# Kernel tuning notes

Measured on AMD Instinct MI355X. Metric: run time of the kernel, lower is better.

## Reference

```python
import jax, jax.numpy as jnp
import numpy as np

N_NODES = 50000
N_EDGES = 640000
N_REL = 200
D_IN = 128
D_OUT = 128


def setup_inputs() -> dict:
    key = jax.random.key(0)
    k1, k2, k3, k4, k5, k6 = jax.random.split(key, 6)
    x = jax.random.normal(k1, (N_NODES, D_IN), dtype=jnp.float32)
    edge_index = jax.random.randint(k2, (2, N_EDGES), 0, N_NODES, dtype=jnp.int64)
    edge_type = jax.random.randint(k3, (N_EDGES,), 0, N_REL, dtype=jnp.int64)
    rel_emb = jax.random.normal(k4, (N_REL, D_IN), dtype=jnp.float32)
    # nn.Linear weights stored as [out_features, in_features]
    W_lin = jax.random.normal(k5, (D_OUT, D_IN), dtype=jnp.float32) * (1.0 / np.sqrt(D_IN))
    # xavier_uniform for attn kernel [1, D_IN]
    limit = np.sqrt(6.0 / (1 + D_IN))
    W_attn = jax.random.uniform(k6, (1, D_IN), dtype=jnp.float32, minval=-limit, maxval=limit)
    return {"x": x, "edge_index": edge_index, "edge_type": edge_type,
            "rel_emb": rel_emb, "W_lin": W_lin, "W_attn": W_attn}


def reference(x, edge_index, edge_type, rel_emb, W_lin, W_attn):
    # x: [N, D_in]; edge_index: [2, E]; edge_type: [E]; rel_emb: [R, D_in]
    x_trans = x @ W_lin.T                       # [N, D_out]
    src_idx, tgt_idx = edge_index[0], edge_index[1]
    h_src = x[src_idx]                          # [E, D_in] gather
    h_rel = rel_emb[edge_type]                  # [E, D_in] gather
    sum_feat = h_src + h_rel                    # [E, D_in]
    attn = jax.nn.sigmoid(sum_feat @ W_attn.T)  # [E, 1]
    msg = x_trans[src_idx] * attn               # [E, D_out]
    out = jax.ops.segment_sum(msg, tgt_idx, num_segments=x.shape[0])  # [N, D_out]
    return jax.nn.relu(out)
```

## Files before the change

kernel.cpp:

```cpp
#include <hip/hip_runtime.h>
#include <hip/hip_bf16.h>

#define N_NODES 50000
#define N_EDGES 640000
#define N_REL   200
#define D       128
#define CAP     64
#define RANGES  8
#define NODES_PER_RANGE (N_NODES / RANGES)
#define CHUNK_EDGES 2560
#define N_CHUNKS (N_EDGES / CHUNK_EDGES)

typedef __attribute__((ext_vector_type(8))) short short8;
typedef __attribute__((ext_vector_type(4))) float floatx4;

__device__ __forceinline__ unsigned short f2bf(float f) {
    unsigned u = __float_as_uint(f);
    u += 0x7FFF + ((u >> 16) & 1);
    return (unsigned short)(u >> 16);
}

__device__ __forceinline__ float sigmoidf(float x) {
    return 1.f / (1.f + __expf(-x));
}

__global__ void setup_kernel(const float* __restrict__ W,
                             const float* __restrict__ x,
                             const float* __restrict__ rel,
                             const float* __restrict__ Wattn,
                             unsigned short* __restrict__ Wbf,
                             float* __restrict__ s_rel,
                             float* __restrict__ s_node,
                             int* __restrict__ count) {
    const int b = blockIdx.x;
    if (b < 64) {
        const int i = b * 256 + threadIdx.x;
        Wbf[i] = f2bf(W[i]);
    } else if (b < 114) {
        const int wave = (b - 64) * 4 + (threadIdx.x >> 6);
        const int lane = threadIdx.x & 63;
        if (wave < N_REL) {
            const float* __restrict__ row = rel + (size_t)wave * D;
            float a = fmaf(row[lane], Wattn[lane],
                           row[lane + 64] * Wattn[lane + 64]);
#pragma unroll
            for (int off = 32; off; off >>= 1)
                a += __shfl_down(a, off);
            if (lane == 0) s_rel[wave] = a;
        }
    } else if (b < 310) {
        const int i = (b - 114) * 256 + threadIdx.x;
        if (i < N_NODES) count[i] = 0;
    } else {
        const int node = (b - 310) * 8 + (threadIdx.x >> 5);
        const int sub  = threadIdx.x & 31;
        if (node < N_NODES) {
            const float4 xv = ((const float4*)(x + (size_t)node * D))[sub];
            const float4 wv = ((const float4*)Wattn)[sub];
            float a = xv.x * wv.x + xv.y * wv.y + xv.z * wv.z + xv.w * wv.w;
#pragma unroll
            for (int off = 16; off; off >>= 1)
                a += __shfl_xor(a, off);
            if (sub == 0) s_node[node] = a;
        }
    }
}

__global__ void xtrans_mfma_kernel(const float* __restrict__ x,
                                   const unsigned short* __restrict__ Wbf,
                                   unsigned short* __restrict__ xt) {
    const int wid = (blockIdx.x * blockDim.x + threadIdx.x) >> 6;
    if (wid >= N_NODES / 16) return;
    const int lane = threadIdx.x & 63;
    const int r16  = lane & 15;
    const int quad = lane >> 4;
    const int m0   = wid * 16;

    short8 af[4];
#pragma unroll
    for (int s = 0; s < 4; ++s) {
        const int k0 = s * 32 + quad * 8;
        const float* __restrict__ xr = x + (size_t)(m0 + r16) * D + k0;
        const float4 lo = *(const float4*)(xr);
        const float4 hi = *(const float4*)(xr + 4);
        short8 a;
        a[0] = (short)f2bf(lo.x); a[1] = (short)f2bf(lo.y);
        a[2] = (short)f2bf(lo.z); a[3] = (short)f2bf(lo.w);
        a[4] = (short)f2bf(hi.x); a[5] = (short)f2bf(hi.y);
        a[6] = (short)f2bf(hi.z); a[7] = (short)f2bf(hi.w);
        af[s] = a;
    }

#pragma unroll
    for (int t = 0; t < 8; ++t) {
        floatx4 acc = {0.f, 0.f, 0.f, 0.f};
#pragma unroll
        for (int s = 0; s < 4; ++s) {
            const int k0 = s * 32 + quad * 8;
            const short8 b = *(const short8*)(Wbf + (size_t)(t * 16 + r16) * D + k0);
            acc = __builtin_amdgcn_mfma_f32_16x16x32_bf16(af[s], b, acc, 0, 0, 0);
        }
#pragma unroll
        for (int r = 0; r < 4; ++r) {
            const int orow = m0 + quad * 4 + r;
            xt[(size_t)orow * D + t * 16 + r16] = f2bf(acc[r]);
        }
    }
}

__global__ void scatter_kernel(const int* __restrict__ src_idx,
                               const int* __restrict__ tgt_idx,
                               const int* __restrict__ etype,
                               const float* __restrict__ s_node,
                               const float* __restrict__ s_rel,
                               int* __restrict__ count,
                               unsigned* __restrict__ sorted) {
    const int b     = blockIdx.x;
    const int lo    = (b & 7) * NODES_PER_RANGE;
    const int hi    = lo + NODES_PER_RANGE;
    const int base  = (b >> 3) * CHUNK_EDGES + threadIdx.x;

#pragma unroll
    for (int it = 0; it < CHUNK_EDGES / 256; ++it) {
        const int e = base + it * 256;
        const int t = tgt_idx[e];
        if (t >= lo && t < hi) {
            const int s = src_idx[e];
            const int r = etype[e];
            const float logit = s_node[s] + s_rel[r];
            const unsigned rec =
                ((unsigned)f2bf(sigmoidf(logit)) << 16) | (unsigned)s;
            const int k = atomicAdd(&count[t], 1);
            sorted[t * CAP + k] = rec;
        }
    }
}

__device__ __forceinline__ void gproc(unsigned r, const unsigned short* __restrict__ xt,
                                      int sub, float4& acc) {
    const unsigned src = r & 0xFFFFu;
    const float a = __uint_as_float(r & 0xFFFF0000u);
    const uint2 p = *(const uint2*)(xt + (size_t)src * D + sub * 4);
    acc.x = fmaf(a, __uint_as_float(p.x << 16),        acc.x);
    acc.y = fmaf(a, __uint_as_float(p.x & 0xFFFF0000u), acc.y);
    acc.z = fmaf(a, __uint_as_float(p.y << 16),        acc.z);
    acc.w = fmaf(a, __uint_as_float(p.y & 0xFFFF0000u), acc.w);
}

__global__ void gather_kernel(const int* __restrict__ count,
                              const unsigned* __restrict__ sorted,
                              const unsigned short* __restrict__ xt,
                              float* __restrict__ out) {
    const int wid  = (blockIdx.x * blockDim.x + threadIdx.x) >> 6;
    const int lane = threadIdx.x & 63;
    const int half = lane >> 5;
    const int sub  = lane & 31;
    const int t    = wid * 2 + half;
    if (t >= N_NODES) return;

    const int cnt = count[t];
    const unsigned* __restrict__ rec = sorted + (size_t)t * CAP;

    float4 acc = {0.f, 0.f, 0.f, 0.f};
    int i = 0;
    for (; i + 4 <= cnt; i += 4) {
        const uint4 r4 = *(const uint4*)(rec + i);
        gproc(r4.x, xt, sub, acc);
        gproc(r4.y, xt, sub, acc);
        gproc(r4.z, xt, sub, acc);
        gproc(r4.w, xt, sub, acc);
    }
    for (; i < cnt; ++i)
        gproc(rec[i], xt, sub, acc);

    float4 o;
    o.x = fmaxf(acc.x, 0.f);
    o.y = fmaxf(acc.y, 0.f);
    o.z = fmaxf(acc.z, 0.f);
    o.w = fmaxf(acc.w, 0.f);
    ((float4*)(out + (size_t)t * D))[sub] = o;
}

extern "C" void kernel_launch(void* const* d_in, const int* in_sizes, int n_in,
                              void* d_out, int out_size, void* d_ws, size_t ws_size,
                              hipStream_t stream) {
    const float* x        = (const float*)d_in[0];
    const int*   edge_idx = (const int*)d_in[1];
    const int*   etype    = (const int*)d_in[2];
    const float* rel_emb  = (const float*)d_in[3];
    const float* W_lin    = (const float*)d_in[4];
    const float* W_attn   = (const float*)d_in[5];
    float* out = (float*)d_out;

    const int* src_idx = edge_idx;
    const int* tgt_idx = edge_idx + N_EDGES;

    unsigned short* xt   = (unsigned short*)d_ws;
    float* s_node        = (float*)(xt + (size_t)N_NODES * D);
    float* s_rel         = s_node + N_NODES;
    unsigned short* Wbf  = (unsigned short*)(s_rel + N_REL);
    int*   count         = (int*)(Wbf + D * D);
    unsigned* sorted     = (unsigned*)(count + N_NODES);

    setup_kernel<<<dim3(310 + (N_NODES + 7) / 8), dim3(256), 0, stream>>>(
        W_lin, x, rel_emb, W_attn, Wbf, s_rel, s_node, count);

    xtrans_mfma_kernel<<<dim3((N_NODES / 16 * 64 + 255) / 256), dim3(256), 0, stream>>>(
        x, Wbf, xt);

    scatter_kernel<<<dim3(N_CHUNKS * RANGES), dim3(256), 0, stream>>>(
        src_idx, tgt_idx, etype, s_node, s_rel, count, sorted);

    gather_kernel<<<dim3(N_NODES / 8), dim3(256), 0, stream>>>(
        count, sorted, xt, out);
}
```

Baseline: 167.1 us.

## Fuse x-transform GEMM and edge scatter into one interleaved launch

Merges the bf16 MFMA x·W^T kernel and the edge scatter/bucketing kernel into a single launch. Block groups are interleaved proportionally, so compute-heavy GEMM blocks and atomic-heavy scatter blocks run concurrently and one kernel launch and its tail are removed. It also switches edge-index, record reads and output stores to nontemporal loads and stores to reduce cache pollution. The interleaving mapping adds a little index arithmetic and may change occupancy balance.

```diff
diff --git a/kernel.cpp b/kernel.cpp
--- a/kernel.cpp
+++ b/kernel.cpp
@@ -11,8 +11,14 @@
 #define CHUNK_EDGES 2560
 #define N_CHUNKS (N_EDGES / CHUNK_EDGES)
 
+#define XT_WAVES   (N_NODES / 16)
+#define XT_GROUPS  98
+#define SC_GROUPS  N_CHUNKS
+#define TOT_GROUPS (XT_GROUPS + SC_GROUPS)
+
 typedef __attribute__((ext_vector_type(8))) short short8;
 typedef __attribute__((ext_vector_type(4))) float floatx4;
+typedef __attribute__((ext_vector_type(4))) unsigned uintx4;
 
 __device__ __forceinline__ unsigned short f2bf(float f) {
     unsigned u = __float_as_uint(f);
@@ -24,14 +30,15 @@
     return 1.f / (1.f + __expf(-x));
 }
 
-__global__ void setup_kernel(const float* __restrict__ W,
-                             const float* __restrict__ x,
-                             const float* __restrict__ rel,
-                             const float* __restrict__ Wattn,
-                             unsigned short* __restrict__ Wbf,
-                             float* __restrict__ s_rel,
-                             float* __restrict__ s_node,
-                             int* __restrict__ count) {
+__global__ __launch_bounds__(256) void setup_kernel(
+        const float* __restrict__ W,
+        const float* __restrict__ x,
+        const float* __restrict__ rel,
+        const float* __restrict__ Wattn,
+        unsigned short* __restrict__ Wbf,
+        float* __restrict__ s_rel,
+        float* __restrict__ s_node,
+        int* __restrict__ count) {
     const int b = blockIdx.x;
     if (b < 64) {
         const int i = b * 256 + threadIdx.x;
@@ -66,91 +73,99 @@
     }
 }
 
-__global__ void xtrans_mfma_kernel(const float* __restrict__ x,
-                                   const unsigned short* __restrict__ Wbf,
-                                   unsigned short* __restrict__ xt) {
-    const int wid = (blockIdx.x * blockDim.x + threadIdx.x) >> 6;
-    if (wid >= N_NODES / 16) return;
-    const int lane = threadIdx.x & 63;
-    const int r16  = lane & 15;
-    const int quad = lane >> 4;
-    const int m0   = wid * 16;
-
-    short8 af[4];
-#pragma unroll
-    for (int s = 0; s < 4; ++s) {
-        const int k0 = s * 32 + quad * 8;
-        const float* __restrict__ xr = x + (size_t)(m0 + r16) * D + k0;
-        const float4 lo = *(const float4*)(xr);
-        const float4 hi = *(const float4*)(xr + 4);
-        short8 a;
-        a[0] = (short)f2bf(lo.x); a[1] = (short)f2bf(lo.y);
-        a[2] = (short)f2bf(lo.z); a[3] = (short)f2bf(lo.w);
-        a[4] = (short)f2bf(hi.x); a[5] = (short)f2bf(hi.y);
-        a[6] = (short)f2bf(hi.z); a[7] = (short)f2bf(hi.w);
-        af[s] = a;
-    }
-
-#pragma unroll
-    for (int t = 0; t < 8; ++t) {
-        floatx4 acc = {0.f, 0.f, 0.f, 0.f};
+__global__ __launch_bounds__(256) void fused_kernel(
+        const float* __restrict__ x,
+        const unsigned short* __restrict__ Wbf,
+        unsigned short* __restrict__ xt,
+        const int* __restrict__ src_idx,
+        const int* __restrict__ tgt_idx,
+        const int* __restrict__ etype,
+        const float* __restrict__ s_node,
+        const float* __restrict__ s_rel,
+        int* __restrict__ count,
+        unsigned* __restrict__ sorted) {
+    const int g    = blockIdx.x >> 3;
+    const int sub8 = blockIdx.x & 7;
+    const int xg   = (g * XT_GROUPS) / TOT_GROUPS;
+    const bool is_x = (((g + 1) * XT_GROUPS) / TOT_GROUPS) > xg;
+
+    if (is_x) {
+        const int wid = (xg * 8 + sub8) * 4 + (threadIdx.x >> 6);
+        if (wid >= XT_WAVES) return;
+        const int lane = threadIdx.x & 63;
+        const int r16  = lane & 15;
+        const int quad = lane >> 4;
+        const int m0   = wid * 16;
+
+        short8 af[4];
 #pragma unroll
         for (int s = 0; s < 4; ++s) {
             const int k0 = s * 32 + quad * 8;
-            const short8 b = *(const short8*)(Wbf + (size_t)(t * 16 + r16) * D + k0);
-            acc = __builtin_amdgcn_mfma_f32_16x16x32_bf16(af[s], b, acc, 0, 0, 0);
-        }
-#pragma unroll
-        for (int r = 0; r < 4; ++r) {
-            const int orow = m0 + quad * 4 + r;
-            xt[(size_t)orow * D + t * 16 + r16] = f2bf(acc[r]);
+            const float* __restrict__ xr = x + (size_t)(m0 + r16) * D + k0;
+            const float4 lo = *(const float4*)(xr);
+            const float4 hi = *(const float4*)(xr + 4);
+            short8 a;
+            a[0] = (short)f2bf(lo.x); a[1] = (short)f2bf(lo.y);
+            a[2] = (short)f2bf(lo.z); a[3] = (short)f2bf(lo.w);
+            a[4] = (short)f2bf(hi.x); a[5] = (short)f2bf(hi.y);
+            a[6] = (short)f2bf(hi.z); a[7] = (short)f2bf(hi.w);
+            af[s] = a;
+        }
+
+#pragma unroll
+        for (int t = 0; t < 8; ++t) {
+            floatx4 acc = {0.f, 0.f, 0.f, 0.f};
+#pragma unroll
+            for (int s = 0; s < 4; ++s) {
+                const int k0 = s * 32 + quad * 8;
+                const short8 bfr = *(const short8*)(Wbf + (size_t)(t * 16 + r16) * D + k0);
+                acc = __builtin_amdgcn_mfma_f32_16x16x32_bf16(af[s], bfr, acc, 0, 0, 0);
+            }
+#pragma unroll
+            for (int r = 0; r < 4; ++r) {
+                const int orow = m0 + quad * 4 + r;
+                xt[(size_t)orow * D + t * 16 + r16] = f2bf(acc[r]);
+            }
+        }
+    } else {
+        const int sg   = g - xg;
+        const int lo   = sub8 * NODES_PER_RANGE;
+        const int hi   = lo + NODES_PER_RANGE;
+        const int base = sg * CHUNK_EDGES + threadIdx.x;
+
+#pragma unroll
+        for (int it = 0; it < CHUNK_EDGES / 256; ++it) {
+            const int e = base + it * 256;
+            const int t = __builtin_nontemporal_load(tgt_idx + e);
+            if (t >= lo && t < hi) {
+                const int s = __builtin_nontemporal_load(src_idx + e);
+                const int r = __builtin_nontemporal_load(etype + e);
+                const float logit = s_node[s] + s_rel[r];
+                const unsigned rec =
+                    ((unsigned)f2bf(sigmoidf(logit)) << 16) | (unsigned)s;
+                const int k = atomicAdd(&count[t], 1);
+                sorted[t * CAP + k] = rec;
+            }
         }
     }
 }
 
-__global__ void scatter_kernel(const int* __restrict__ src_idx,
-                               const int* __restrict__ tgt_idx,
-                               const int* __restrict__ etype,
-                               const float* __restrict__ s_node,
-                               const float* __restrict__ s_rel,
-                               int* __restrict__ count,
-                               unsigned* __restrict__ sorted) {
-    const int b     = blockIdx.x;
-    const int lo    = (b & 7) * NODES_PER_RANGE;
-    const int hi    = lo + NODES_PER_RANGE;
-    const int base  = (b >> 3) * CHUNK_EDGES + threadIdx.x;
-
-#pragma unroll
-    for (int it = 0; it < CHUNK_EDGES / 256; ++it) {
-        const int e = base + it * 256;
-        const int t = tgt_idx[e];
-        if (t >= lo && t < hi) {
-            const int s = src_idx[e];
-            const int r = etype[e];
-            const float logit = s_node[s] + s_rel[r];
-            const unsigned rec =
-                ((unsigned)f2bf(sigmoidf(logit)) << 16) | (unsigned)s;
-            const int k = atomicAdd(&count[t], 1);
-            sorted[t * CAP + k] = rec;
-        }
-    }
-}
-
 __device__ __forceinline__ void gproc(unsigned r, const unsigned short* __restrict__ xt,
-                                      int sub, float4& acc) {
+                                      int sub, floatx4& acc) {
     const unsigned src = r & 0xFFFFu;
     const float a = __uint_as_float(r & 0xFFFF0000u);
     const uint2 p = *(const uint2*)(xt + (size_t)src * D + sub * 4);
-    acc.x = fmaf(a, __uint_as_float(p.x << 16),        acc.x);
-    acc.y = fmaf(a, __uint_as_float(p.x & 0xFFFF0000u), acc.y);
-    acc.z = fmaf(a, __uint_as_float(p.y << 16),        acc.z);
-    acc.w = fmaf(a, __uint_as_float(p.y & 0xFFFF0000u), acc.w);
-}
-
-__global__ void gather_kernel(const int* __restrict__ count,
-                              const unsigned* __restrict__ sorted,
-                              const unsigned short* __restrict__ xt,
-                              float* __restrict__ out) {
+    acc[0] = fmaf(a, __uint_as_float(p.x << 16),         acc[0]);
+    acc[1] = fmaf(a, __uint_as_float(p.x & 0xFFFF0000u), acc[1]);
+    acc[2] = fmaf(a, __uint_as_float(p.y << 16),         acc[2]);
+    acc[3] = fmaf(a, __uint_as_float(p.y & 0xFFFF0000u), acc[3]);
+}
+
+__global__ __launch_bounds__(256) void gather_kernel(
+        const int* __restrict__ count,
+        const unsigned* __restrict__ sorted,
+        const unsigned short* __restrict__ xt,
+        float* __restrict__ out) {
     const int wid  = (blockIdx.x * blockDim.x + threadIdx.x) >> 6;
     const int lane = threadIdx.x & 63;
     const int half = lane >> 5;
@@ -161,24 +176,24 @@
     const int cnt = count[t];
     const unsigned* __restrict__ rec = sorted + (size_t)t * CAP;
 
-    float4 acc = {0.f, 0.f, 0.f, 0.f};
+    floatx4 acc = {0.f, 0.f, 0.f, 0.f};
     int i = 0;
     for (; i + 4 <= cnt; i += 4) {
-        const uint4 r4 = *(const uint4*)(rec + i);
+        const uintx4 r4 = __builtin_nontemporal_load((const uintx4*)(rec + i));
         gproc(r4.x, xt, sub, acc);
         gproc(r4.y, xt, sub, acc);
         gproc(r4.z, xt, sub, acc);
         gproc(r4.w, xt, sub, acc);
     }
     for (; i < cnt; ++i)
-        gproc(rec[i], xt, sub, acc);
-
-    float4 o;
-    o.x = fmaxf(acc.x, 0.f);
-    o.y = fmaxf(acc.y, 0.f);
-    o.z = fmaxf(acc.z, 0.f);
-    o.w = fmaxf(acc.w, 0.f);
-    ((float4*)(out + (size_t)t * D))[sub] = o;
+        gproc(__builtin_nontemporal_load(rec + i), xt, sub, acc);
+
+    floatx4 o;
+    o[0] = fmaxf(acc[0], 0.f);
+    o[1] = fmaxf(acc[1], 0.f);
+    o[2] = fmaxf(acc[2], 0.f);
+    o[3] = fmaxf(acc[3], 0.f);
+    __builtin_nontemporal_store(o, (floatx4*)(out + (size_t)t * D) + sub);
 }
 
 extern "C" void kernel_launch(void* const* d_in, const int* in_sizes, int n_in,
@@ -205,11 +220,8 @@
     setup_kernel<<<dim3(310 + (N_NODES + 7) / 8), dim3(256), 0, stream>>>(
         W_lin, x, rel_emb, W_attn, Wbf, s_rel, s_node, count);
 
-    xtrans_mfma_kernel<<<dim3((N_NODES / 16 * 64 + 255) / 256), dim3(256), 0, stream>>>(
-        x, Wbf, xt);
-
-    scatter_kernel<<<dim3(N_CHUNKS * RANGES), dim3(256), 0, stream>>>(
-        src_idx, tgt_idx, etype, s_node, s_rel, count, sorted);
+    fused_kernel<<<dim3(TOT_GROUPS * 8), dim3(256), 0, stream>>>(
+        x, Wbf, xt, src_idx, tgt_idx, etype, s_node, s_rel, count, sorted);
 
     gather_kernel<<<dim3(N_NODES / 8), dim3(256), 0, stream>>>(
         count, sorted, xt, out);
```

Measured after the change: 178.9 us. +7.1%, slower.
